# Performance work log

Hardware: AMD Instinct MI355X
Metric: run time of the kernel (lower is better)

The kernel has to match this reference:

```python
import jax, jax.numpy as jnp
import numpy as np

N_NODES = 100_000
N_EDGES = 3_200_000
D_IN, D_EDGE, D_HID, D_OUT = 8, 4, 32, 16
NEG_SLOPE = 0.2  # PyG GATv2Conv default


def setup_inputs() -> dict:
    key = jax.random.key(0)
    ks = jax.random.split(key, 13)
    s = 0.1
    return {
        "x": jax.random.normal(ks[0], (N_NODES, D_IN), jnp.float32),
        "edge_index": jax.random.randint(ks[1], (2, N_EDGES), 0, N_NODES, dtype=jnp.int64),
        "edge_attr": jax.random.normal(ks[2], (N_EDGES, D_EDGE), jnp.float32),
        "Wl1": jax.random.normal(ks[3], (D_IN, D_HID), jnp.float32) * s,
        "Wr1": jax.random.normal(ks[4], (D_IN, D_HID), jnp.float32) * s,
        "We1": jax.random.normal(ks[5], (D_EDGE, D_HID), jnp.float32) * s,
        "att1": jax.random.normal(ks[6], (D_HID,), jnp.float32) * s,
        "b1": jnp.zeros((D_HID,), jnp.float32),
        "Wl2": jax.random.normal(ks[7], (D_HID, D_OUT), jnp.float32) * s,
        "Wr2": jax.random.normal(ks[8], (D_HID, D_OUT), jnp.float32) * s,
        "We2": jax.random.normal(ks[9], (D_EDGE, D_OUT), jnp.float32) * s,
        "att2": jax.random.normal(ks[10], (D_OUT,), jnp.float32) * s,
        "b2": jnp.zeros((D_OUT,), jnp.float32),
    }


def _segment_softmax(score, seg, n):
    m = jax.ops.segment_max(score, seg, num_segments=n)
    e = jnp.exp(score - m[seg])
    z = jax.ops.segment_sum(e, seg, num_segments=n)
    return e / z[seg]


def _gatv2(x, src, dst, ea_raw, Wl, Wr, We, att, bias, n):
    # GATv2 (heads=1): score_ij = att . leaky_relu(Wl x_j + Wr x_i + We e_ij)
    xl = x @ Wl            # [N, d]
    xr = x @ Wr            # [N, d]
    ea = ea_raw @ We       # [E, d]
    h = jax.nn.leaky_relu(xl[src] + xr[dst] + ea, NEG_SLOPE)  # [E, d]
    score = h @ att        # [E]
    alpha = _segment_softmax(score, dst, n)
    out = jax.ops.segment_sum(alpha[:, None] * xl[src], dst, num_segments=n)
    return out + bias


def reference(x, edge_index, edge_attr, Wl1, Wr1, We1, att1, b1, Wl2, Wr2, We2, att2, b2):
    n = x.shape[0]
    src, dst = edge_index[0], edge_index[1]
    # add_self_loops=True with fill_value='mean': self-loop edge_attr = mean of
    # incoming raw edge_attr per target node (0 for isolated targets)
    ones = jnp.ones((src.shape[0],), x.dtype)
    cnt = jax.ops.segment_sum(ones, dst, num_segments=n)
    loop_attr = jax.ops.segment_sum(edge_attr, dst, num_segments=n) / jnp.maximum(cnt, 1.0)[:, None]
    ar = jnp.arange(n, dtype=src.dtype)
    src2 = jnp.concatenate([src, ar])
    dst2 = jnp.concatenate([dst, ar])
    ea2 = jnp.concatenate([edge_attr, loop_attr], axis=0)
    h = jax.nn.relu(_gatv2(x, src2, dst2, ea2, Wl1, Wr1, We1, att1, b1, n))
    out = _gatv2(h, src2, dst2, ea2, Wl2, Wr2, We2, att2, b2, n)
    return out.reshape(-1)
```

## Files before the change

### kernel.cpp

```cpp
#include <hip/hip_runtime.h>

#define NEG_SLOPE 0.2f
#define CHUNK 4096
#define KMAX  512
#define NBLKMAX 1024
#define CAPB  9472

__global__ __launch_bounds__(1024) void k_bin(const int* __restrict__ ei,
                                              const float* __restrict__ eattr,
                                              int* __restrict__ cloff,
                                              int* __restrict__ ssrc,
                                              float4* __restrict__ seat,
                                              int E, int K) {
    __shared__ int s_off[KMAX + 1];
    __shared__ int s_scan[1024];
    __shared__ int s_ssrc[CHUNK];
    __shared__ float4 s_seat[CHUNK];
    int t = threadIdx.x;
    for (int i = t; i <= K; i += 1024) s_off[i] = 0;
    __syncthreads();
    int base = blockIdx.x * CHUNK;
    int Ec = min(CHUNK, E - base);
    unsigned pack[CHUNK / 1024];
#pragma unroll
    for (int i = 0; i < CHUNK / 1024; i++) {
        int el = t + 1024 * i;
        pack[i] = 0xFFFFFFFFu;
        if (el < Ec) {
            int dst = ei[E + base + el];
            int b = dst >> 8;
            int r = atomicAdd(&s_off[b], 1);
            pack[i] = ((unsigned)b << 20) | ((unsigned)(dst & 255) << 12) | (unsigned)r;
        }
    }
    __syncthreads();
    int x0 = (t <= K) ? s_off[t] : 0;
    s_scan[t] = x0;
    __syncthreads();
    for (int off = 1; off < 1024; off <<= 1) {
        int y = (t >= off) ? s_scan[t - off] : 0;
        __syncthreads();
        s_scan[t] += y;
        __syncthreads();
    }
    if (t <= K) s_off[t] = s_scan[t] - x0;
    __syncthreads();
#pragma unroll
    for (int i = 0; i < CHUNK / 1024; i++) {
        int el = t + 1024 * i;
        if (el < Ec) {
            unsigned p = pack[i];
            int b = p >> 20;
            int dl = (p >> 12) & 255;
            int r = p & 0xFFF;
            int pos = s_off[b] + r;
            int e = base + el;
            s_ssrc[pos] = ei[e] | (dl << 17);
            s_seat[pos] = *(const float4*)(eattr + 4ll * e);
        }
    }
    __syncthreads();
    for (int pos = t; pos < Ec; pos += 1024) {
        ssrc[base + pos] = s_ssrc[pos];
        seat[base + pos] = s_seat[pos];
    }
    for (int i = t; i <= K; i += 1024)
        cloff[(long long)blockIdx.x * (K + 1) + i] = s_off[i];
}

__global__ void k_transp(const int* __restrict__ in, int* __restrict__ out, int R, int C) {
    __shared__ int tile[32][33];
    int c0 = blockIdx.x * 32, r0 = blockIdx.y * 32;
    int c = c0 + threadIdx.x, r = r0 + threadIdx.y;
    if (r < R && c < C) tile[threadIdx.y][threadIdx.x] = in[(long long)r * C + c];
    __syncthreads();
    int oc = r0 + threadIdx.x, orr = c0 + threadIdx.y;
    if (orr < C && oc < R) out[(long long)orr * R + oc] = tile[threadIdx.x][threadIdx.y];
}

__global__ void k_btot(const int* __restrict__ cloffT, int* __restrict__ bucketTotal,
                       int K, int NBLK) {
    int b = (blockIdx.x * blockDim.x + threadIdx.x) >> 6;
    int lane = threadIdx.x & 63;
    if (b >= K) return;
    const int* r0 = cloffT + (long long)b * NBLK;
    const int* r1 = r0 + NBLK;
    int s = 0;
    for (int c = lane; c < NBLK; c += 64) s += r1[c] - r0[c];
#pragma unroll
    for (int off = 32; off >= 1; off >>= 1) s += __shfl_xor(s, off, 64);
    if (lane == 0) bucketTotal[b] = s;
}

__global__ void k_scanK(const int* __restrict__ bucketTotal, int* __restrict__ slotBase,
                        int* __restrict__ qofs, int N, int K) {
    __shared__ int s[512];
    int t = threadIdx.x;
    int v[4];
    int sum = 0;
    int base = t * 4;
    for (int j = 0; j < 4; j++) {
        int b = base + j, x = 0;
        if (b < K) { int nb = min(256, N - (b << 8)); x = bucketTotal[b] + nb; }
        v[j] = sum;
        sum += x;
    }
    s[t] = sum;
    __syncthreads();
    for (int off = 1; off < 512; off <<= 1) {
        int x = (t >= off) ? s[t - off] : 0;
        __syncthreads();
        s[t] += x;
        __syncthreads();
    }
    int tb = s[t] - sum;
    for (int j = 0; j < 4; j++) {
        int b = base + j;
        if (b < K) slotBase[b] = tb + v[j];
    }
    if (t == 511) { slotBase[K] = s[511]; qofs[4ll * N] = s[511]; }
}

__global__ __launch_bounds__(1024, 1) void k_perm(const int* __restrict__ ssrc,
                                                  const float4* __restrict__ seat,
                                                  const int* __restrict__ cloffT,
                                                  const int* __restrict__ slotBase,
                                                  int* __restrict__ qofs,
                                                  int* __restrict__ fsrc,
                                                  float4* __restrict__ feat,
                                                  int N, int K, int NBLK, int QDIV) {
    __shared__ int co[NBLKMAX], qq[NBLKMAX + 1], sc[NBLKMAX];
    __shared__ int hist2[1024], cur2[1024], lst2[1024], sc2[1024];
    __shared__ int hist[256];
    __shared__ float lsum[256][4];
    __shared__ int s_p[CAPB];
    __shared__ int s_inv[CAPB];
    int b = blockIdx.x, t = threadIdx.x;
    int nb = min(256, N - (b << 8));
    hist2[t] = 0; cur2[t] = 0;
    if (t < 256) { lsum[t][0] = 0.f; lsum[t][1] = 0.f; lsum[t][2] = 0.f; lsum[t][3] = 0.f; }
    const int* r0 = cloffT + (long long)b * NBLK;
    const int* r1 = r0 + NBLK;
    int len = 0;
    if (t < NBLK) { int c0v = r0[t]; len = r1[t] - c0v; co[t] = c0v; }
    sc[t] = (t < NBLK) ? len : 0;
    __syncthreads();
    for (int off = 1; off < NBLKMAX; off <<= 1) {
        int x = (t >= off) ? sc[t - off] : 0;
        __syncthreads();
        sc[t] += x;
        __syncthreads();
    }
    if (t < NBLK) qq[t] = sc[t] - len;
    if (t == NBLKMAX - 1) qq[NBLK] = sc[NBLKMAX - 1];
    __syncthreads();
    int Eb = qq[NBLK];
    for (int i = t; i < Eb; i += 1024) {
        int lo2 = 0, hi2 = NBLK;
        while (lo2 + 1 < hi2) { int mid = (lo2 + hi2) >> 1; if (qq[mid] <= i) lo2 = mid; else hi2 = mid; }
        int g = lo2 * CHUNK + co[lo2] + (i - qq[lo2]);
        int p = ssrc[g];
        s_p[i] = p;
        int q = (int)((unsigned)(p & 0x1FFFF) / (unsigned)QDIV);
        atomicAdd(&hist2[(((p >> 17) & 255) << 2) | q], 1);
    }
    __syncthreads();
    if (t < 256) {
        int c = hist2[4 * t] + hist2[4 * t + 1] + hist2[4 * t + 2] + hist2[4 * t + 3];
        hist[t] = c;
        if (t < nb) {
            int node = (b << 8) + t;
            int qs = (int)((unsigned)node / (unsigned)QDIV);
            hist2[4 * t + qs] += 1;
            cur2[4 * t + qs] = 1;
        }
    }
    __syncthreads();
    sc2[t] = hist2[t];
    __syncthreads();
    for (int off = 1; off < 1024; off <<= 1) {
        int x = (t >= off) ? sc2[t - off] : 0;
        __syncthreads();
        sc2[t] += x;
        __syncthreads();
    }
    lst2[t] = sc2[t] - hist2[t];
    __syncthreads();
    int lo = slotBase[b];
    if (t < 4 * nb) qofs[((long long)b << 10) + t] = lo + lst2[t];
    if (t < nb) {
        int node = (b << 8) + t;
        int qs = (int)((unsigned)node / (unsigned)QDIV);
        s_inv[lst2[4 * t + qs]] = -(t + 1);
    }
    __syncthreads();
    for (int i = t; i < Eb; i += 1024) {
        int p = s_p[i];
        int q = (int)((unsigned)(p & 0x1FFFF) / (unsigned)QDIV);
        int bin = (((p >> 17) & 255) << 2) | q;
        int r = atomicAdd(&cur2[bin], 1);
        s_inv[lst2[bin] + r] = i;
    }
    __syncthreads();
    int tot = Eb + nb;
    for (int pos = t; pos < tot; pos += 1024) {
        int i2 = s_inv[pos];
        if (i2 >= 0) {
            int p = s_p[i2];
            int lo2 = 0, hi2 = NBLK;
            while (lo2 + 1 < hi2) { int mid = (lo2 + hi2) >> 1; if (qq[mid] <= i2) lo2 = mid; else hi2 = mid; }
            int g = lo2 * CHUNK + co[lo2] + (i2 - qq[lo2]);
            float4 a = seat[g];
            long long gp = lo + pos;
            fsrc[gp] = p & 0x1FFFF;
            feat[gp] = a;
            int dl = (p >> 17) & 255;
            atomicAdd(&lsum[dl][0], a.x);
            atomicAdd(&lsum[dl][1], a.y);
            atomicAdd(&lsum[dl][2], a.z);
            atomicAdd(&lsum[dl][3], a.w);
        }
    }
    __syncthreads();
    if (t < nb) {
        int node = (b << 8) + t;
        int qs = (int)((unsigned)node / (unsigned)QDIV);
        float inv = 1.f / fmaxf((float)hist[t], 1.f);
        long long pos = lo + lst2[4 * t + qs];
        fsrc[pos] = node;
        feat[pos] = make_float4(lsum[t][0] * inv, lsum[t][1] * inv,
                                lsum[t][2] * inv, lsum[t][3] * inv);
    }
}

template <int DIN, int D>
__global__ void k_xform(const float* __restrict__ x, const float* __restrict__ Wl,
                        const float* __restrict__ Wr, float* __restrict__ xl,
                        float* __restrict__ xr, int N) {
    __shared__ float sWl[DIN * D], sWr[DIN * D];
    for (int i = threadIdx.x; i < DIN * D; i += blockDim.x) { sWl[i] = Wl[i]; sWr[i] = Wr[i]; }
    __syncthreads();
    int t = blockIdx.x * blockDim.x + threadIdx.x;
    if (t >= N * D) return;
    int n = t / D, d = t % D;
    const float* xp = x + (long long)n * DIN;
    float sl = 0.f, sr = 0.f;
#pragma unroll
    for (int k = 0; k < DIN; k++) {
        float xv = xp[k];
        sl += xv * sWl[k * D + d];
        sr += xv * sWr[k * D + d];
    }
    xl[t] = sl;
    xr[t] = sr;
}

template <int L>
__device__ __forceinline__ void gat_edge(bool valid, const float4& a, const float4& xlv,
                                         const float4& we0, const float4& we1,
                                         const float4& we2, const float4& we3,
                                         const float4& av, const float4& xrv,
                                         float4& acc, float& z) {
    float4 v;
    v.x = fmaf(a.x, we0.x, xrv.x); v.x = fmaf(a.y, we1.x, v.x);
    v.x = fmaf(a.z, we2.x, v.x);   v.x = fmaf(a.w, we3.x, v.x); v.x += xlv.x;
    v.y = fmaf(a.x, we0.y, xrv.y); v.y = fmaf(a.y, we1.y, v.y);
    v.y = fmaf(a.z, we2.y, v.y);   v.y = fmaf(a.w, we3.y, v.y); v.y += xlv.y;
    v.z = fmaf(a.x, we0.z, xrv.z); v.z = fmaf(a.y, we1.z, v.z);
    v.z = fmaf(a.z, we2.z, v.z);   v.z = fmaf(a.w, we3.z, v.z); v.z += xlv.z;
    v.w = fmaf(a.x, we0.w, xrv.w); v.w = fmaf(a.y, we1.w, v.w);
    v.w = fmaf(a.z, we2.w, v.w);   v.w = fmaf(a.w, we3.w, v.w); v.w += xlv.w;
    v.x = v.x > 0.f ? v.x : NEG_SLOPE * v.x;
    v.y = v.y > 0.f ? v.y : NEG_SLOPE * v.y;
    v.z = v.z > 0.f ? v.z : NEG_SLOPE * v.z;
    v.w = v.w > 0.f ? v.w : NEG_SLOPE * v.w;
    float sc = av.x * v.x + av.y * v.y + av.z * v.z + av.w * v.w;
#pragma unroll
    for (int off = L / 2; off >= 1; off >>= 1) sc += __shfl_xor(sc, off, 64);
    float ev = valid ? __expf(sc) : 0.f;
    z += ev;
    acc.x = fmaf(ev, xlv.x, acc.x);
    acc.y = fmaf(ev, xlv.y, acc.y);
    acc.z = fmaf(ev, xlv.z, acc.z);
    acc.w = fmaf(ev, xlv.w, acc.w);
}

template <int D, bool RELU>
__global__ void k_gat(const int* __restrict__ fsrc,
                      const float4* __restrict__ feat,
                      const int* __restrict__ qofs,
                      const float* __restrict__ xl, const float* __restrict__ xr,
                      const float* __restrict__ We, const float* __restrict__ att,
                      const float* __restrict__ bias, float* __restrict__ out, int N) {
    constexpr int L = D / 4;
    constexpr int G = 64 / L;
    int w = (blockIdx.x * blockDim.x + threadIdx.x) >> 6;
    int lane = threadIdx.x & 63;
    if (w >= N) return;
    int g = lane / L;
    int j = lane % L;
    int s0 = qofs[4 * w], s1 = qofs[4 * w + 4];
    int cnt = s1 - s0;

    const float4 we0 = *(const float4*)(We + 0 * D + 4 * j);
    const float4 we1 = *(const float4*)(We + 1 * D + 4 * j);
    const float4 we2 = *(const float4*)(We + 2 * D + 4 * j);
    const float4 we3 = *(const float4*)(We + 3 * D + 4 * j);
    const float4 av  = *(const float4*)(att + 4 * j);
    const float4 xrv = *(const float4*)(xr + (long long)w * D + 4 * j);

    float4 acc = make_float4(0.f, 0.f, 0.f, 0.f);
    float z = 0.f;

    int it = 0;
    for (; (it + 2) * G <= cnt; it += 2) {
        int sl = s0 + it * G + g;
        int srcA = fsrc[sl];
        int srcB = fsrc[sl + G];
        float4 aA = feat[sl];
        float4 aB = feat[sl + G];
        float4 xA = *(const float4*)(xl + (long long)srcA * D + 4 * j);
        float4 xB = *(const float4*)(xl + (long long)srcB * D + 4 * j);
        gat_edge<L>(true, aA, xA, we0, we1, we2, we3, av, xrv, acc, z);
        gat_edge<L>(true, aB, xB, we0, we1, we2, we3, av, xrv, acc, z);
    }
    for (; it * G < cnt; ++it) {
        int o = it * G + g;
        bool v = o < cnt;
        int sl = s0 + min(o, cnt - 1);
        int src = fsrc[sl];
        float4 a = feat[sl];
        float4 xv = *(const float4*)(xl + (long long)src * D + 4 * j);
        gat_edge<L>(v, a, xv, we0, we1, we2, we3, av, xrv, acc, z);
    }

#pragma unroll
    for (int off = 32; off >= L; off >>= 1) {
        acc.x += __shfl_xor(acc.x, off, 64);
        acc.y += __shfl_xor(acc.y, off, 64);
        acc.z += __shfl_xor(acc.z, off, 64);
        acc.w += __shfl_xor(acc.w, off, 64);
        z += __shfl_xor(z, off, 64);
    }

    if (g == 0) {
        float inv = 1.0f / z;
        float4 bv = *(const float4*)(bias + 4 * j);
        float4 o;
        o.x = acc.x * inv + bv.x;
        o.y = acc.y * inv + bv.y;
        o.z = acc.z * inv + bv.z;
        o.w = acc.w * inv + bv.w;
        if (RELU) {
            o.x = fmaxf(o.x, 0.f); o.y = fmaxf(o.y, 0.f);
            o.z = fmaxf(o.z, 0.f); o.w = fmaxf(o.w, 0.f);
        }
        *(float4*)(out + (long long)w * D + 4 * j) = o;
    }
}

extern "C" void kernel_launch(void* const* d_in, const int* in_sizes, int n_in,
                              void* d_out, int out_size, void* d_ws, size_t ws_size,
                              hipStream_t stream) {
    const float* x     = (const float*)d_in[0];
    const int*   ei    = (const int*)d_in[1];
    const float* eattr = (const float*)d_in[2];
    const float* Wl1   = (const float*)d_in[3];
    const float* Wr1   = (const float*)d_in[4];
    const float* We1   = (const float*)d_in[5];
    const float* att1  = (const float*)d_in[6];
    const float* b1    = (const float*)d_in[7];
    const float* Wl2   = (const float*)d_in[8];
    const float* Wr2   = (const float*)d_in[9];
    const float* We2   = (const float*)d_in[10];
    const float* att2  = (const float*)d_in[11];
    const float* b2    = (const float*)d_in[12];

    const int N = in_sizes[0] / 8;
    const int E = in_sizes[1] / 2;
    const int K = (N + 255) >> 8;
    const int NBLK = (E + CHUNK - 1) / CHUNK;
    const int QDIV = (N + 3) / 4;

    int* iws = (int*)d_ws;
    size_t o = 0;
    int* bucketTotal = iws + o; o += K;
    int* slotBase    = iws + o; o += K + 1;
    int* qofs        = iws + o; o += 4ll * N + 1;
    int* cloff       = iws + o; o += (size_t)NBLK * (K + 1);
    int* cloffT      = iws + o; o += (size_t)(K + 1) * NBLK;
    o = (o + 7) & ~(size_t)7;
    int*    fsrc = (int*)(iws + o);    o += (size_t)(E + N);
    o = (o + 3) & ~(size_t)3;
    float4* feat = (float4*)(iws + o); o += 4ll * (E + N);
    size_t stage = o;
    int*    ssrc = (int*)(iws + o);    o += (size_t)E;
    o = (o + 3) & ~(size_t)3;
    float4* seat = (float4*)(iws + o); o += 4ll * E;
    float* xl = (float*)(iws + stage);
    float* xr = xl + 32ll * N;
    float* h  = xr + 32ll * N;

    const int B = 256;
    auto cdiv = [](long long a, long long b) { return (int)((a + b - 1) / b); };

    k_bin<<<NBLK, 1024, 0, stream>>>(ei, eattr, cloff, ssrc, seat, E, K);
    dim3 tb(32, 32);
    k_transp<<<dim3(cdiv(K + 1, 32), cdiv(NBLK, 32)), tb, 0, stream>>>(cloff, cloffT, NBLK, K + 1);
    k_btot<<<cdiv(64ll * K, B), B, 0, stream>>>(cloffT, bucketTotal, K, NBLK);
    k_scanK<<<1, 512, 0, stream>>>(bucketTotal, slotBase, qofs, N, K);
    k_perm<<<K, 1024, 0, stream>>>(ssrc, seat, cloffT, slotBase, qofs, fsrc, feat, N, K, NBLK, QDIV);

    k_xform<8, 32><<<cdiv(32ll * N, B), B, 0, stream>>>(x, Wl1, Wr1, xl, xr, N);
    k_gat<32, true><<<cdiv(N, 4), B, 0, stream>>>(fsrc, feat, qofs, xl, xr, We1, att1, b1, h, N);

    k_xform<32, 16><<<cdiv(16ll * N, B), B, 0, stream>>>(h, Wl2, Wr2, xl, xr, N);
    k_gat<16, false><<<cdiv(N, 4), B, 0, stream>>>(fsrc, feat, qofs, xl, xr, We2, att2, b2, (float*)d_out, N);
}
```

Measured before the change: 499.7 us.

## Drop s_p shared buffer in k_perm to fit two blocks per CU

Removes the s_p shared-memory array from the permutation kernel. The source ids are now re-read from global memory, with the binary search recomputed in the scatter pass, and s_inv stores global indices directly. This cuts LDS use so launch bounds can allow two 1024-thread blocks per CU. The final gather loop is also unrolled by two to keep more loads in flight, at the cost of extra global reads and a repeated binary search.

```diff
diff --git a/kernel.cpp b/kernel.cpp
--- a/kernel.cpp
+++ b/kernel.cpp
@@ -121,7 +121,7 @@
     if (t == 511) { slotBase[K] = s[511]; qofs[4ll * N] = s[511]; }
 }
 
-__global__ __launch_bounds__(1024, 1) void k_perm(const int* __restrict__ ssrc,
+__global__ __launch_bounds__(1024, 2) void k_perm(const int* __restrict__ ssrc,
                                                   const float4* __restrict__ seat,
                                                   const int* __restrict__ cloffT,
                                                   const int* __restrict__ slotBase,
@@ -133,7 +133,6 @@
     __shared__ int hist2[1024], cur2[1024], lst2[1024], sc2[1024];
     __shared__ int hist[256];
     __shared__ float lsum[256][4];
-    __shared__ int s_p[CAPB];
     __shared__ int s_inv[CAPB];
     int b = blockIdx.x, t = threadIdx.x;
     int nb = min(256, N - (b << 8));
@@ -160,7 +159,6 @@
         while (lo2 + 1 < hi2) { int mid = (lo2 + hi2) >> 1; if (qq[mid] <= i) lo2 = mid; else hi2 = mid; }
         int g = lo2 * CHUNK + co[lo2] + (i - qq[lo2]);
         int p = ssrc[g];
-        s_p[i] = p;
         int q = (int)((unsigned)(p & 0x1FFFF) / (unsigned)QDIV);
         atomicAdd(&hist2[(((p >> 17) & 255) << 2) | q], 1);
     }
@@ -195,30 +193,55 @@
     }
     __syncthreads();
     for (int i = t; i < Eb; i += 1024) {
-        int p = s_p[i];
+        int lo2 = 0, hi2 = NBLK;
+        while (lo2 + 1 < hi2) { int mid = (lo2 + hi2) >> 1; if (qq[mid] <= i) lo2 = mid; else hi2 = mid; }
+        int g = lo2 * CHUNK + co[lo2] + (i - qq[lo2]);
+        int p = ssrc[g];
         int q = (int)((unsigned)(p & 0x1FFFF) / (unsigned)QDIV);
         int bin = (((p >> 17) & 255) << 2) | q;
         int r = atomicAdd(&cur2[bin], 1);
-        s_inv[lst2[bin] + r] = i;
+        s_inv[lst2[bin] + r] = g;
     }
     __syncthreads();
     int tot = Eb + nb;
-    for (int pos = t; pos < tot; pos += 1024) {
-        int i2 = s_inv[pos];
-        if (i2 >= 0) {
-            int p = s_p[i2];
-            int lo2 = 0, hi2 = NBLK;
-            while (lo2 + 1 < hi2) { int mid = (lo2 + hi2) >> 1; if (qq[mid] <= i2) lo2 = mid; else hi2 = mid; }
-            int g = lo2 * CHUNK + co[lo2] + (i2 - qq[lo2]);
+    int pos = t;
+    for (; pos + 1024 < tot; pos += 2048) {
+        int gA = s_inv[pos];
+        int gB = s_inv[pos + 1024];
+        bool vA = gA >= 0, vB = gB >= 0;
+        int cA = vA ? gA : 0, cB = vB ? gB : 0;
+        int pA = ssrc[cA];
+        int pB = ssrc[cB];
+        float4 aA = seat[cA];
+        float4 aB = seat[cB];
+        if (vA) {
+            long long gp = lo + pos;
+            fsrc[gp] = pA & 0x1FFFF;
+            feat[gp] = aA;
+            int dl = (pA >> 17) & 255;
+            atomicAdd(&lsum[dl][0], aA.x); atomicAdd(&lsum[dl][1], aA.y);
+            atomicAdd(&lsum[dl][2], aA.z); atomicAdd(&lsum[dl][3], aA.w);
+        }
+        if (vB) {
+            long long gp = lo + pos + 1024;
+            fsrc[gp] = pB & 0x1FFFF;
+            feat[gp] = aB;
+            int dl = (pB >> 17) & 255;
+            atomicAdd(&lsum[dl][0], aB.x); atomicAdd(&lsum[dl][1], aB.y);
+            atomicAdd(&lsum[dl][2], aB.z); atomicAdd(&lsum[dl][3], aB.w);
+        }
+    }
+    for (; pos < tot; pos += 1024) {
+        int g = s_inv[pos];
+        if (g >= 0) {
+            int p = ssrc[g];
             float4 a = seat[g];
             long long gp = lo + pos;
             fsrc[gp] = p & 0x1FFFF;
             feat[gp] = a;
             int dl = (p >> 17) & 255;
-            atomicAdd(&lsum[dl][0], a.x);
-            atomicAdd(&lsum[dl][1], a.y);
-            atomicAdd(&lsum[dl][2], a.z);
-            atomicAdd(&lsum[dl][3], a.w);
+            atomicAdd(&lsum[dl][0], a.x); atomicAdd(&lsum[dl][1], a.y);
+            atomicAdd(&lsum[dl][2], a.z); atomicAdd(&lsum[dl][3], a.w);
         }
     }
     __syncthreads();
@@ -226,10 +249,10 @@
         int node = (b << 8) + t;
         int qs = (int)((unsigned)node / (unsigned)QDIV);
         float inv = 1.f / fmaxf((float)hist[t], 1.f);
-        long long pos = lo + lst2[4 * t + qs];
-        fsrc[pos] = node;
-        feat[pos] = make_float4(lsum[t][0] * inv, lsum[t][1] * inv,
-                                lsum[t][2] * inv, lsum[t][3] * inv);
+        long long pos2 = lo + lst2[4 * t + qs];
+        fsrc[pos2] = node;
+        feat[pos2] = make_float4(lsum[t][0] * inv, lsum[t][1] * inv,
+                                 lsum[t][2] * inv, lsum[t][3] * inv);
     }
 }
 
```

After: 490.4 us. About the same (-1.9%).
